# Kernel tuning notes

Measured on AMD Instinct MI355X. Metric: run time of the kernel, lower is better.

Reference implementation:

```python
import jax, jax.numpy as jnp
import numpy as np

N_NODES = 100000
N_EDGES = 2000000


def _init_mlp(key, dims, scale=0.05):
    Ws, bs = [], []
    ks = jax.random.split(key, len(dims) - 1)
    for k, di, do in zip(ks, dims[:-1], dims[1:]):
        Ws.append(jax.random.normal(k, (di, do), dtype=jnp.float32) * scale)
        bs.append(jnp.zeros((do,), dtype=jnp.float32))
    return Ws, bs


def setup_inputs() -> dict:
    key = jax.random.key(0)
    ks = jax.random.split(key, 7)
    d = {
        "t": jax.random.uniform(ks[0], (1,), dtype=jnp.float32),
        "x": jax.random.normal(ks[1], (N_NODES, 4), dtype=jnp.float32),
        "Ofixed": jax.random.normal(ks[2], (N_NODES, 2), dtype=jnp.float32),
        "src_idx": jax.random.randint(ks[3], (N_EDGES,), 0, N_NODES, dtype=jnp.int32),
        "tgt_idx": jax.random.randint(ks[4], (N_EDGES,), 0, N_NODES, dtype=jnp.int32),
    }
    # fR: (2*d_O+1)=13 -> [150]*4 -> 50 ; fO: 50 -> [100] -> 4
    R_Ws, R_bs = _init_mlp(ks[5], [13, 150, 150, 150, 150, 50])
    O_Ws, O_bs = _init_mlp(ks[6], [50, 100, 4])
    for i, (W, b) in enumerate(zip(R_Ws, R_bs)):
        d[f"fR_W{i}"] = W
        d[f"fR_b{i}"] = b
    for i, (W, b) in enumerate(zip(O_Ws, O_bs)):
        d[f"fO_W{i}"] = W
        d[f"fO_b{i}"] = b
    return d


def _mlp(h, Ws, bs):
    # hidden layers with ReLU, linear output (matches MLP in the torch code)
    for W, b in zip(Ws[:-1], bs[:-1]):
        h = jax.nn.relu(h @ W + b)
    return h @ Ws[-1] + bs[-1]


def reference(t, x, Ofixed, src_idx, tgt_idx,
              fR_W0, fR_b0, fR_W1, fR_b1, fR_W2, fR_b2, fR_W3, fR_b3, fR_W4, fR_b4,
              fO_W0, fO_b0, fO_W1, fO_b1):
    O = jnp.concatenate([x, Ofixed], axis=1)            # [N, d_O]
    # Msrc.T @ O and Mtgt.T @ O with 0/1 incidence matrices == gathers
    Rsrc = O[src_idx]                                   # [M, d_O]
    Rtgt = O[tgt_idx]                                   # [M, d_O]
    tt = jnp.broadcast_to(t.reshape(1, 1).astype(O.dtype), (src_idx.shape[0], 1))
    R_prime = jnp.concatenate([Rsrc, Rtgt, tt], axis=1)  # [M, 2*d_O+1]
    E = _mlp(R_prime, [fR_W0, fR_W1, fR_W2, fR_W3, fR_W4],
             [fR_b0, fR_b1, fR_b2, fR_b3, fR_b4])        # [M, d_E]
    # Mtgt @ E == scatter-add of edge messages onto target nodes
    E_prime = jax.ops.segment_sum(E, tgt_idx, num_segments=x.shape[0])  # [N, d_E]
    P = _mlp(E_prime, [fO_W0, fO_W1], [fO_b0, fO_b1])    # [N, d_P]
    return P
```

## Files before the change

kernel.cpp:

```cpp
#include <hip/hip_runtime.h>
#include <hip/hip_bf16.h>

typedef unsigned short u16;
typedef unsigned int u32;
typedef __attribute__((ext_vector_type(8))) short short8;
typedef __attribute__((ext_vector_type(4))) float f32x4;

constexpr int SA     = 192;
constexpr int BLK_E  = 64;
constexpr int NTHR   = 256;
constexpr int CHUNK  = 512;
constexpr int WSLOT  = 50 * CHUNK;
constexpr size_t WS_HDR   = 262144;

constexpr int Ls (int s) { return s == 0 ? 0 : (s <= 15 ? 1 + (s - 1) / 5 : 4); }
constexpr int Kss(int s) { return s == 0 ? 0 : (s <= 15 ? (s - 1) % 5 : s - 16); }

__device__ __forceinline__ int aswz(int row, int elem) {
    return row * SA + (elem ^ ((row & 7) << 3));
}

__device__ __forceinline__ u16 f2bf(float f) {
    union { float f; unsigned u; } c; c.f = f;
    return (u16)((c.u + 0x7fffu + ((c.u >> 16) & 1u)) >> 16);
}
__device__ __forceinline__ unsigned pk_bf16(float a, float b) {
    float2 f; f.x = a; f.y = b;
    __hip_bfloat162 h = __float22bfloat162_rn(f);
    return *(unsigned*)&h;
}

__device__ __forceinline__ int kperm(int kp) {
    if (kp < 64)  return (kp & 3) * 16 + (kp >> 2);
    if (kp < 128) { const int m = kp - 64; return (5 + (m & 3)) * 16 + (m >> 2); }
    if (kp < 144) return 4 * 16 + (kp - 128);
    if (kp < 160) return 9 * 16 + (kp - 144);
    return 1 << 30;
}

__global__ void prep_all(const float* __restrict__ W0, const float* __restrict__ W1,
                         const float* __restrict__ W2, const float* __restrict__ W3,
                         const float* __restrict__ W4,
                         const float* __restrict__ B0, const float* __restrict__ B1,
                         const float* __restrict__ B2, const float* __restrict__ B3,
                         const float* __restrict__ B4,
                         u16* __restrict__ Wt)
{
    const int l = blockIdx.y;
    const float* W; const float* B; int DI, DO; bool perm;
    if      (l == 0) { W = W0; B = B0; DI = 13;  DO = 150; perm = false; }
    else if (l == 1) { W = W1; B = B1; DI = 150; DO = 150; perm = true;  }
    else if (l == 2) { W = W2; B = B2; DI = 150; DO = 150; perm = true;  }
    else if (l == 3) { W = W3; B = B3; DI = 150; DO = 150; perm = true;  }
    else             { W = W4; B = B4; DI = 150; DO = 50;  perm = true;  }
    const int kbias = (l == 0) ? 13 : 150;
    u16* dst = Wt + (size_t)l * WSLOT;
    for (int idx = blockIdx.x * blockDim.x + threadIdx.x; idx < WSLOT;
         idx += gridDim.x * blockDim.x) {
        const int chunk = idx / CHUNK;
        const int within = idx - chunk * CHUNK;
        const int lane = within >> 3, e = within & 7;
        const int ks = chunk / 10, j = chunk - ks * 10;
        const int c = lane & 15, q = lane >> 4;
        const int n = j * 16 + c;
        const int kphys = ks * 32 + q * 8 + e;
        const int klog = perm ? kperm(kphys) : kphys;
        float v = 0.f;
        if (n < DO) {
            if (klog < DI)          v = W[klog * DO + n];
            else if (klog == kbias) v = B[n];
        }
        dst[idx] = f2bf(v);
    }
}

__device__ __forceinline__ void loadB(const u16* __restrict__ Wt, int s,
                                      int ng, int lane, short8 (&slot)[5])
{
    const int l = Ls(s), ks = Kss(s);
    const int jb = (l < 4) ? ng * 5 : 0;
    const int nt = (l < 4) ? 5 : 4;
    const u16* base = Wt + (size_t)l * WSLOT + (size_t)(ks * 10 + jb) * CHUNK + lane * 8;
#pragma unroll
    for (int jj = 0; jj < 5; ++jj)
        if (jj < nt) slot[jj] = *(const short8*)&base[jj * CHUNK];
}

__device__ __forceinline__ void epilogue(u16* act, int mg, int ng, int col, int quad,
                                         f32x4 (&acc)[2][5])
{
#pragma unroll
    for (int mtl = 0; mtl < 2; ++mtl)
#pragma unroll
        for (int r = 0; r < 4; ++r) {
            const int row = (mg * 2 + mtl) * 16 + quad * 4 + r;
            uint2 pk;
            pk.x = pk_bf16(fmaxf(acc[mtl][0][r], 0.f), fmaxf(acc[mtl][1][r], 0.f));
            pk.y = pk_bf16(fmaxf(acc[mtl][2][r], 0.f), fmaxf(acc[mtl][3][r], 0.f));
            *(uint2*)&act[aswz(row, ng * 64 + col * 4)] = pk;
            u16 sv = (u16)pk_bf16(fmaxf(acc[mtl][4][r], 0.f), 0.f);
            if (ng == 1 && col == 6) sv = 0x3F80;
            act[aswz(row, 128 + ng * 16 + col)] = sv;
        }
}

__global__ void hist_kernel(const int* __restrict__ tgt, u32* __restrict__ cnt,
                            int n_edges)
{
    const int e = blockIdx.x * blockDim.x + threadIdx.x;
    if (e < n_edges) atomicAdd(&cnt[tgt[e]], 1u);
}

__global__ void scan1_kernel(const u32* __restrict__ cnt, u32* __restrict__ offs,
                             u32* __restrict__ bsum, int n)
{
    __shared__ u32 s[256];
    const int i = blockIdx.x * 256 + threadIdx.x;
    const u32 v = (i < n) ? cnt[i] : 0u;
    s[threadIdx.x] = v; __syncthreads();
#pragma unroll
    for (int d = 1; d < 256; d <<= 1) {
        const u32 t = (threadIdx.x >= d) ? s[threadIdx.x - d] : 0u;
        __syncthreads();
        s[threadIdx.x] += t;
        __syncthreads();
    }
    if (i < n) offs[i] = s[threadIdx.x] - v;
    if (threadIdx.x == 255) bsum[blockIdx.x] = s[255];
}

__global__ void scan2_kernel(u32* __restrict__ bsum, int nb)
{
    __shared__ u32 s[512];
    const int i = threadIdx.x;
    const u32 v = (i < nb) ? bsum[i] : 0u;
    s[i] = v; __syncthreads();
#pragma unroll
    for (int d = 1; d < 512; d <<= 1) {
        const u32 t = (i >= d) ? s[i - d] : 0u;
        __syncthreads();
        s[i] += t;
        __syncthreads();
    }
    if (i < nb) bsum[i] = s[i] - v;
}

__global__ void scan3_kernel(u32* __restrict__ offs, const u32* __restrict__ bsum,
                             u32* __restrict__ cursor, int n, int n_edges)
{
    const int i = blockIdx.x * 256 + threadIdx.x;
    if (i < n) {
        const u32 o = offs[i] + bsum[blockIdx.x];
        offs[i] = o;
        cursor[i] = o;
    }
    if (blockIdx.x == 0 && threadIdx.x == 0) offs[n] = (u32)n_edges;
}

__global__ void perm_kernel(const int* __restrict__ src, const int* __restrict__ tgt,
                            u32* __restrict__ cursor, int2* __restrict__ sg,
                            int n_edges)
{
    const int e = blockIdx.x * blockDim.x + threadIdx.x;
    if (e < n_edges) {
        const int g = tgt[e];
        const u32 pos = atomicAdd(&cursor[g], 1u);
        sg[pos] = make_int2(src[e], g);
    }
}

__global__ __launch_bounds__(NTHR, 4) void edge_kernel(
    const float* __restrict__ t, const float* __restrict__ x, const float* __restrict__ Ofx,
    const int2* __restrict__ sgp,
    const u16* __restrict__ Wt,
    float* __restrict__ Ep, int n_edges)
{
    __shared__ __align__(16) u16 act[BLK_E * SA];
    __shared__ int tgt_s[BLK_E];

    const int tid  = threadIdx.x;
    const int lane = tid & 63;
    const int wv   = tid >> 6;
    const int mg   = wv >> 1;
    const int ng   = wv & 1;
    const int col  = lane & 15;
    const int quad = lane >> 4;

    short8 Bwin[2][5];
    loadB(Wt, 0, ng, lane, Bwin[0]);
    loadB(Wt, 1, ng, lane, Bwin[1]);

    if (lane < 16) {
        const int e = wv * 16 + lane;
        const long long ge = (long long)blockIdx.x * BLK_E + e;
        const bool valid = ge < n_edges;
        const int2 sg = valid ? sgp[ge] : make_int2(0, 0);
        const int s = sg.x;
        const int g = valid ? sg.y : -1;
        const float4 xs = valid ? *(const float4*)&x[(size_t)s * 4] : float4{0, 0, 0, 0};
        const float2 os = valid ? *(const float2*)&Ofx[(size_t)s * 2] : float2{0, 0};
        const float4 xg = valid ? *(const float4*)&x[(size_t)sg.y * 4] : float4{0, 0, 0, 0};
        const float2 og = valid ? *(const float2*)&Ofx[(size_t)sg.y * 2] : float2{0, 0};
        const float tv = valid ? t[0] : 0.f;
        uint4 w0, w1;
        w0.x = pk_bf16(xs.x, xs.y); w0.y = pk_bf16(xs.z, xs.w);
        w0.z = pk_bf16(os.x, os.y); w0.w = pk_bf16(xg.x, xg.y);
        w1.x = pk_bf16(xg.z, xg.w); w1.y = pk_bf16(og.x, og.y);
        w1.z = pk_bf16(tv, 1.0f);   w1.w = 0u;
        *(uint4*)&act[aswz(e, 0)]  = w0;
        *(uint4*)&act[aswz(e, 8)]  = w1;
        *(uint4*)&act[aswz(e, 16)] = uint4{0, 0, 0, 0};
        *(uint4*)&act[aswz(e, 24)] = uint4{0, 0, 0, 0};
        tgt_s[e] = g;
    }
    __syncthreads();

    const f32x4 z = {0.f, 0.f, 0.f, 0.f};
    f32x4 acc[2][5];
    short8 Af[2];

#pragma unroll
    for (int mtl = 0; mtl < 2; ++mtl)
        Af[mtl] = *(const short8*)&act[aswz((mg * 2 + mtl) * 16 + col, quad * 8)];
#pragma unroll
    for (int jj = 0; jj < 5; ++jj)
#pragma unroll
        for (int mtl = 0; mtl < 2; ++mtl)
            acc[mtl][jj] = __builtin_amdgcn_mfma_f32_16x16x32_bf16(
                Af[mtl], Bwin[0][jj], z, 0, 0, 0);
    loadB(Wt, 2, ng, lane, Bwin[0]);
    __syncthreads();
    epilogue(act, mg, ng, col, quad, acc);
    __syncthreads();

#pragma unroll
    for (int s = 1; s <= 15; ++s) {
        const int ks = (s - 1) % 5;
        const int slot = s & 1;
#pragma unroll
        for (int mtl = 0; mtl < 2; ++mtl)
            Af[mtl] = *(const short8*)&act[aswz((mg * 2 + mtl) * 16 + col,
                                                ks * 32 + quad * 8)];
#pragma unroll
        for (int jj = 0; jj < 5; ++jj)
#pragma unroll
            for (int mtl = 0; mtl < 2; ++mtl) {
                if (ks == 0)
                    acc[mtl][jj] = __builtin_amdgcn_mfma_f32_16x16x32_bf16(
                        Af[mtl], Bwin[slot][jj], z, 0, 0, 0);
                else
                    acc[mtl][jj] = __builtin_amdgcn_mfma_f32_16x16x32_bf16(
                        Af[mtl], Bwin[slot][jj], acc[mtl][jj], 0, 0, 0);
            }
        if (s + 2 <= 20) loadB(Wt, s + 2, ng, lane, Bwin[slot]);
        if (ks == 4) {
            __syncthreads();
            epilogue(act, mg, ng, col, quad, acc);
            __syncthreads();
        }
    }

    const int mt4 = mg * 2 + ng;
    f32x4 acc4[4];
#pragma unroll
    for (int s = 16; s <= 20; ++s) {
        const int ks = s - 16;
        const int slot = s & 1;
        const short8 A4 = *(const short8*)&act[aswz(mt4 * 16 + col,
                                                    ks * 32 + quad * 8)];
#pragma unroll
        for (int jj = 0; jj < 4; ++jj) {
            if (ks == 0)
                acc4[jj] = __builtin_amdgcn_mfma_f32_16x16x32_bf16(
                    A4, Bwin[slot][jj], z, 0, 0, 0);
            else
                acc4[jj] = __builtin_amdgcn_mfma_f32_16x16x32_bf16(
                    A4, Bwin[slot][jj], acc4[jj], 0, 0, 0);
        }
        if (s + 2 <= 20) loadB(Wt, s + 2, ng, lane, Bwin[slot]);
    }

    __syncthreads();
    float* actF = (float*)act;
#pragma unroll
    for (int jj = 0; jj < 4; ++jj) {
        const int n = jj * 16 + col;
        if (n < 50) {
#pragma unroll
            for (int r = 0; r < 4; ++r)
                actF[(mt4 * 16 + quad * 4 + r) * 52 + n] = acc4[jj][r];
        }
    }
    __syncthreads();
    if (tid < 200) {
        const int h = tid / 50;
        const int c = tid - h * 50;
        const int r0 = h * 16;
        int   cur = tgt_s[r0];
        float a   = 0.f;
        for (int r = r0; r < r0 + 16; ++r) {
            const int   g = tgt_s[r];
            const float v = actF[r * 52 + c];
            if (g != cur) {
                if (cur >= 0) atomicAdd(&Ep[(size_t)cur * 50 + c], a);
                a = 0.f; cur = g;
            }
            a += v;
        }
        if (cur >= 0) atomicAdd(&Ep[(size_t)cur * 50 + c], a);
    }
}

template<int DI, int DO, bool RELU>
__device__ __forceinline__ void mlp_layer_t(
    const float* __restrict__ W, const float* __restrict__ B,
    float (*in)[64], float (*out)[64], int tid)
{
    const int et = tid & 15;
    const int jt = tid >> 4;
    constexpr int NG = (DO + 15) / 16;

    float acc0[NG], acc1[NG], acc2[NG], acc3[NG];
#pragma unroll
    for (int g = 0; g < NG; ++g) {
        const int j = jt + 16 * g;
        const float bb = (j < DO) ? B[j] : 0.f;
        acc0[g] = bb; acc1[g] = bb; acc2[g] = bb; acc3[g] = bb;
    }
    for (int k = 0; k < DI; ++k) {
        const float4 a = *(const float4*)&in[k][et * 4];
#pragma unroll
        for (int g = 0; g < NG; ++g) {
            const int j = jt + 16 * g;
            const float wv = (j < DO) ? W[k * DO + j] : 0.f;
            acc0[g] = fmaf(a.x, wv, acc0[g]);
            acc1[g] = fmaf(a.y, wv, acc1[g]);
            acc2[g] = fmaf(a.z, wv, acc2[g]);
            acc3[g] = fmaf(a.w, wv, acc3[g]);
        }
    }
#pragma unroll
    for (int g = 0; g < NG; ++g) {
        const int j = jt + 16 * g;
        if (j < DO) {
            float4 v; v.x = acc0[g]; v.y = acc1[g]; v.z = acc2[g]; v.w = acc3[g];
            if (RELU) {
                v.x = fmaxf(v.x, 0.f); v.y = fmaxf(v.y, 0.f);
                v.z = fmaxf(v.z, 0.f); v.w = fmaxf(v.w, 0.f);
            }
            *(float4*)&out[j][et * 4] = v;
        }
    }
}

__global__ __launch_bounds__(256, 2) void node_kernel(
    const float* __restrict__ Ep,
    const float* __restrict__ W0, const float* __restrict__ B0,
    const float* __restrict__ W1, const float* __restrict__ B1,
    float* __restrict__ P, int n_nodes)
{
    __shared__ float bufA[104][64];
    __shared__ float bufB[104][64];
    const int tid = threadIdx.x;
    const int n0  = blockIdx.x * 64;

    for (int idx = tid; idx < 64 * 50; idx += 256) {
        const int e = idx / 50;
        const int k = idx - e * 50;
        const int n = n0 + e;
        bufA[k][e] = (n < n_nodes) ? Ep[(size_t)n * 50 + k] : 0.f;
    }
    __syncthreads();
    mlp_layer_t<50, 100, true >(W0, B0, bufA, bufB, tid); __syncthreads();
    mlp_layer_t<100, 4, false>(W1, B1, bufB, bufA, tid); __syncthreads();
    for (int idx = tid; idx < 64 * 4; idx += 256) {
        const int e = idx & 63;
        const int j = idx >> 6;
        const int n = n0 + e;
        if (n < n_nodes) P[(size_t)n * 4 + j] = bufA[j][e];
    }
}

extern "C" void kernel_launch(void* const* d_in, const int* in_sizes, int n_in,
                              void* d_out, int out_size, void* d_ws, size_t ws_size,
                              hipStream_t stream)
{
    const float* t   = (const float*)d_in[0];
    const float* x   = (const float*)d_in[1];
    const float* Ofx = (const float*)d_in[2];
    const int*   src = (const int*)d_in[3];
    const int*   tgt = (const int*)d_in[4];
    const float* W0  = (const float*)d_in[5];  const float* B0 = (const float*)d_in[6];
    const float* W1  = (const float*)d_in[7];  const float* B1 = (const float*)d_in[8];
    const float* W2  = (const float*)d_in[9];  const float* B2 = (const float*)d_in[10];
    const float* W3  = (const float*)d_in[11]; const float* B3 = (const float*)d_in[12];
    const float* W4  = (const float*)d_in[13]; const float* B4 = (const float*)d_in[14];
    const float* OW0 = (const float*)d_in[15]; const float* OB0 = (const float*)d_in[16];
    const float* OW1 = (const float*)d_in[17]; const float* OB1 = (const float*)d_in[18];

    const int n_nodes = in_sizes[1] / 4;
    const int n_edges = in_sizes[3];

    auto align256 = [](size_t v) { return (v + 255) & ~(size_t)255; };
    char* ws = (char*)d_ws;
    const size_t copy_elems = (size_t)n_nodes * 50;
    size_t o = 0;
    u16*   Wt       = (u16*)(ws + o);  o = WS_HDR;
    float* Ep       = (float*)(ws + o); o = align256(o + copy_elems * sizeof(float));
    u32*   offs     = (u32*)(ws + o);  o = align256(o + (size_t)(n_nodes + 1) * 4);
    u32*   cursor   = (u32*)(ws + o);  o = align256(o + (size_t)n_nodes * 4);
    u32*   bsum     = (u32*)(ws + o);  o = align256(o + 512 * 4);
    int2*  sg_perm  = (int2*)(ws + o); o = align256(o + (size_t)n_edges * 8);

    const int NB  = (n_nodes + 255) / 256;
    const int EBK = (n_edges + 255) / 256;

    prep_all<<<dim3(32, 5), 256, 0, stream>>>(W0, W1, W2, W3, W4,
                                              B0, B1, B2, B3, B4, Wt);
    hipMemsetAsync(Ep, 0, copy_elems * sizeof(float), stream);
    hipMemsetAsync(cursor, 0, (size_t)n_nodes * 4, stream);

    hist_kernel <<<EBK, 256, 0, stream>>>(tgt, cursor, n_edges);
    scan1_kernel<<<NB, 256, 0, stream>>>(cursor, offs, bsum, n_nodes);
    scan2_kernel<<<1, 512, 0, stream>>>(bsum, NB);
    scan3_kernel<<<NB, 256, 0, stream>>>(offs, bsum, cursor, n_nodes, n_edges);
    perm_kernel <<<EBK, 256, 0, stream>>>(src, tgt, cursor, sg_perm, n_edges);

    edge_kernel<<<(n_edges + BLK_E - 1) / BLK_E, NTHR, 0, stream>>>(
        t, x, Ofx, sg_perm, Wt, Ep, n_edges);

    node_kernel<<<(n_nodes + 63) / 64, 256, 0, stream>>>(
        Ep, OW0, OB0, OW1, OB1, (float*)d_out, n_nodes);
}
```

Baseline: 907.2 us.

## Stage MLP weights in LDS via async loads and double edges per block

Each wave previously loaded its own slice of weight tiles from global memory into registers. The kernel now uses global_load_lds to stream each weight k-slice once per block into a double-buffered LDS area that all waves read. The block also grows to 128 edges and 512 threads, so each weight fetch is spread over more edges. In exchange there is a block-wide barrier every k-step and more LDS per block, which can lower occupancy. Correctness also depends on the async LDS writes being complete before the barrier.

```diff
diff --git a/kernel.cpp b/kernel.cpp
--- a/kernel.cpp
+++ b/kernel.cpp
@@ -7,8 +7,8 @@
 typedef __attribute__((ext_vector_type(4))) float f32x4;
 
 constexpr int SA     = 192;
-constexpr int BLK_E  = 64;
-constexpr int NTHR   = 256;
+constexpr int BLK_E  = 128;
+constexpr int NTHR   = 512;
 constexpr int CHUNK  = 512;
 constexpr int WSLOT  = 50 * CHUNK;
 constexpr size_t WS_HDR   = 262144;
@@ -28,6 +28,12 @@
     float2 f; f.x = a; f.y = b;
     __hip_bfloat162 h = __float22bfloat162_rn(f);
     return *(unsigned*)&h;
+}
+
+typedef __attribute__((address_space(3))) u16 as3_u16;
+typedef const __attribute__((address_space(1))) u16 as1_u16;
+__device__ __forceinline__ void async16(u16* lds_dst, const u16* gsrc) {
+    __builtin_amdgcn_global_load_lds((as1_u16*)gsrc, (as3_u16*)lds_dst, 16, 0, 0);
 }
 
 __device__ __forceinline__ int kperm(int kp) {
@@ -74,18 +80,6 @@
     }
 }
 
-__device__ __forceinline__ void loadB(const u16* __restrict__ Wt, int s,
-                                      int ng, int lane, short8 (&slot)[5])
-{
-    const int l = Ls(s), ks = Kss(s);
-    const int jb = (l < 4) ? ng * 5 : 0;
-    const int nt = (l < 4) ? 5 : 4;
-    const u16* base = Wt + (size_t)l * WSLOT + (size_t)(ks * 10 + jb) * CHUNK + lane * 8;
-#pragma unroll
-    for (int jj = 0; jj < 5; ++jj)
-        if (jj < nt) slot[jj] = *(const short8*)&base[jj * CHUNK];
-}
-
 __device__ __forceinline__ void epilogue(u16* act, int mg, int ng, int col, int quad,
                                          f32x4 (&acc)[2][5])
 {
@@ -176,6 +170,7 @@
     float* __restrict__ Ep, int n_edges)
 {
     __shared__ __align__(16) u16 act[BLK_E * SA];
+    __shared__ __align__(16) u16 Bs[2][10 * CHUNK];
     __shared__ int tgt_s[BLK_E];
 
     const int tid  = threadIdx.x;
@@ -185,10 +180,14 @@
     const int ng   = wv & 1;
     const int col  = lane & 15;
     const int quad = lane >> 4;
-
-    short8 Bwin[2][5];
-    loadB(Wt, 0, ng, lane, Bwin[0]);
-    loadB(Wt, 1, ng, lane, Bwin[1]);
+    const int jb   = ng * 5;
+
+    {
+        const u16* base = Wt;
+        async16(&Bs[0][wv * CHUNK], base + wv * CHUNK + lane * 8);
+        if (wv < 2)
+            async16(&Bs[0][(8 + wv) * CHUNK], base + (8 + wv) * CHUNK + lane * 8);
+    }
 
     if (lane < 16) {
         const int e = wv * 16 + lane;
@@ -217,26 +216,25 @@
 
     const f32x4 z = {0.f, 0.f, 0.f, 0.f};
     f32x4 acc[2][5];
-    short8 Af[2];
-
-#pragma unroll
-    for (int mtl = 0; mtl < 2; ++mtl)
-        Af[mtl] = *(const short8*)&act[aswz((mg * 2 + mtl) * 16 + col, quad * 8)];
-#pragma unroll
-    for (int jj = 0; jj < 5; ++jj)
-#pragma unroll
-        for (int mtl = 0; mtl < 2; ++mtl)
-            acc[mtl][jj] = __builtin_amdgcn_mfma_f32_16x16x32_bf16(
-                Af[mtl], Bwin[0][jj], z, 0, 0, 0);
-    loadB(Wt, 2, ng, lane, Bwin[0]);
-    __syncthreads();
-    epilogue(act, mg, ng, col, quad, acc);
-    __syncthreads();
-
-#pragma unroll
-    for (int s = 1; s <= 15; ++s) {
-        const int ks = (s - 1) % 5;
-        const int slot = s & 1;
+    short8 Af[2], Bc[5];
+
+#pragma unroll
+    for (int s = 0; s <= 15; ++s) {
+        const int ks = Kss(s);
+        const bool first = (s == 0) || (ks == 0);
+        const bool last  = (s == 0) || (ks == 4);
+        {
+            const int sn = s + 1;
+            const u16* base = Wt + (size_t)Ls(sn) * WSLOT
+                                 + (size_t)(Kss(sn) * 10) * CHUNK;
+            u16* bd = &Bs[sn & 1][0];
+            async16(&bd[wv * CHUNK], base + wv * CHUNK + lane * 8);
+            if (wv < 2)
+                async16(&bd[(8 + wv) * CHUNK], base + (8 + wv) * CHUNK + lane * 8);
+        }
+#pragma unroll
+        for (int jj = 0; jj < 5; ++jj)
+            Bc[jj] = *(const short8*)&Bs[s & 1][(jb + jj) * CHUNK + lane * 8];
 #pragma unroll
         for (int mtl = 0; mtl < 2; ++mtl)
             Af[mtl] = *(const short8*)&act[aswz((mg * 2 + mtl) * 16 + col,
@@ -245,42 +243,52 @@
         for (int jj = 0; jj < 5; ++jj)
 #pragma unroll
             for (int mtl = 0; mtl < 2; ++mtl) {
-                if (ks == 0)
+                if (first)
                     acc[mtl][jj] = __builtin_amdgcn_mfma_f32_16x16x32_bf16(
-                        Af[mtl], Bwin[slot][jj], z, 0, 0, 0);
+                        Af[mtl], Bc[jj], z, 0, 0, 0);
                 else
                     acc[mtl][jj] = __builtin_amdgcn_mfma_f32_16x16x32_bf16(
-                        Af[mtl], Bwin[slot][jj], acc[mtl][jj], 0, 0, 0);
+                        Af[mtl], Bc[jj], acc[mtl][jj], 0, 0, 0);
             }
-        if (s + 2 <= 20) loadB(Wt, s + 2, ng, lane, Bwin[slot]);
-        if (ks == 4) {
-            __syncthreads();
+        __syncthreads();
+        if (last) {
             epilogue(act, mg, ng, col, quad, acc);
             __syncthreads();
         }
     }
 
-    const int mt4 = mg * 2 + ng;
+    const int mt4 = wv;
     f32x4 acc4[4];
 #pragma unroll
     for (int s = 16; s <= 20; ++s) {
         const int ks = s - 16;
-        const int slot = s & 1;
+        if (s < 20) {
+            const int sn = s + 1;
+            const u16* base = Wt + (size_t)4 * WSLOT
+                                 + (size_t)(Kss(sn) * 10) * CHUNK;
+            u16* bd = &Bs[sn & 1][0];
+            async16(&bd[wv * CHUNK], base + wv * CHUNK + lane * 8);
+            if (wv < 2)
+                async16(&bd[(8 + wv) * CHUNK], base + (8 + wv) * CHUNK + lane * 8);
+        }
+        short8 B4[4];
+#pragma unroll
+        for (int jj = 0; jj < 4; ++jj)
+            B4[jj] = *(const short8*)&Bs[s & 1][jj * CHUNK + lane * 8];
         const short8 A4 = *(const short8*)&act[aswz(mt4 * 16 + col,
                                                     ks * 32 + quad * 8)];
 #pragma unroll
         for (int jj = 0; jj < 4; ++jj) {
             if (ks == 0)
                 acc4[jj] = __builtin_amdgcn_mfma_f32_16x16x32_bf16(
-                    A4, Bwin[slot][jj], z, 0, 0, 0);
+                    A4, B4[jj], z, 0, 0, 0);
             else
                 acc4[jj] = __builtin_amdgcn_mfma_f32_16x16x32_bf16(
-                    A4, Bwin[slot][jj], acc4[jj], 0, 0, 0);
-        }
-        if (s + 2 <= 20) loadB(Wt, s + 2, ng, lane, Bwin[slot]);
-    }
-
-    __syncthreads();
+                    A4, B4[jj], acc4[jj], 0, 0, 0);
+        }
+        __syncthreads();
+    }
+
     float* actF = (float*)act;
 #pragma unroll
     for (int jj = 0; jj < 4; ++jj) {
@@ -292,7 +300,7 @@
         }
     }
     __syncthreads();
-    if (tid < 200) {
+    if (tid < 400) {
         const int h = tid / 50;
         const int c = tid - h * 50;
         const int r0 = h * 16;
```

Measured after the change: 903.6 us. Within noise of the previous version (-0.4%).

## Make each wave own 32 edges with full-width layers, removing block barriers

Applied to the files above, without the earlier changes.

Reorganizes the edge MLP so each wavefront processes its own 32 edges across all 160 output columns, instead of splitting N across wave pairs. This eliminates all __syncthreads between layers, since each wave reads and writes only its own rows in LDS. The block size doubles to 128 edges, and the accumulator count doubles to 20 f32x4 per thread, so launch bounds drop to 3 blocks per SM. Each wave now loads the full weight tiles itself, which doubles per-wave weight traffic and raises register pressure and LDS use.

```diff
diff --git a/kernel.cpp b/kernel.cpp
--- a/kernel.cpp
+++ b/kernel.cpp
@@ -7,7 +7,7 @@
 typedef __attribute__((ext_vector_type(4))) float f32x4;
 
 constexpr int SA     = 192;
-constexpr int BLK_E  = 64;
+constexpr int BLK_E  = 128;
 constexpr int NTHR   = 256;
 constexpr int CHUNK  = 512;
 constexpr int WSLOT  = 50 * CHUNK;
@@ -74,33 +74,37 @@
     }
 }
 
-__device__ __forceinline__ void loadB(const u16* __restrict__ Wt, int s,
-                                      int ng, int lane, short8 (&slot)[5])
-{
-    const int l = Ls(s), ks = Kss(s);
-    const int jb = (l < 4) ? ng * 5 : 0;
-    const int nt = (l < 4) ? 5 : 4;
-    const u16* base = Wt + (size_t)l * WSLOT + (size_t)(ks * 10 + jb) * CHUNK + lane * 8;
+__device__ __forceinline__ void loadHalf(const u16* __restrict__ Wt,
+                                         int l, int ks, int g, int nch,
+                                         int lane, short8* buf)
+{
+    const u16* base = Wt + (size_t)l * WSLOT + (size_t)(ks * 10 + g * 5) * CHUNK
+                         + lane * 8;
 #pragma unroll
     for (int jj = 0; jj < 5; ++jj)
-        if (jj < nt) slot[jj] = *(const short8*)&base[jj * CHUNK];
-}
-
-__device__ __forceinline__ void epilogue(u16* act, int mg, int ng, int col, int quad,
-                                         f32x4 (&acc)[2][5])
+        if (jj < nch) buf[jj] = *(const short8*)&base[jj * CHUNK];
+}
+
+__device__ __forceinline__ void epilogueF(u16* act, int ebase, int col, int quad,
+                                          f32x4 (&acc)[2][10])
 {
 #pragma unroll
     for (int mtl = 0; mtl < 2; ++mtl)
 #pragma unroll
         for (int r = 0; r < 4; ++r) {
-            const int row = (mg * 2 + mtl) * 16 + quad * 4 + r;
-            uint2 pk;
-            pk.x = pk_bf16(fmaxf(acc[mtl][0][r], 0.f), fmaxf(acc[mtl][1][r], 0.f));
-            pk.y = pk_bf16(fmaxf(acc[mtl][2][r], 0.f), fmaxf(acc[mtl][3][r], 0.f));
-            *(uint2*)&act[aswz(row, ng * 64 + col * 4)] = pk;
-            u16 sv = (u16)pk_bf16(fmaxf(acc[mtl][4][r], 0.f), 0.f);
-            if (ng == 1 && col == 6) sv = 0x3F80;
-            act[aswz(row, 128 + ng * 16 + col)] = sv;
+            const int row = ebase + mtl * 16 + quad * 4 + r;
+            uint2 p0, p1;
+            p0.x = pk_bf16(fmaxf(acc[mtl][0][r], 0.f), fmaxf(acc[mtl][1][r], 0.f));
+            p0.y = pk_bf16(fmaxf(acc[mtl][2][r], 0.f), fmaxf(acc[mtl][3][r], 0.f));
+            p1.x = pk_bf16(fmaxf(acc[mtl][5][r], 0.f), fmaxf(acc[mtl][6][r], 0.f));
+            p1.y = pk_bf16(fmaxf(acc[mtl][7][r], 0.f), fmaxf(acc[mtl][8][r], 0.f));
+            *(uint2*)&act[aswz(row, col * 4)]      = p0;
+            *(uint2*)&act[aswz(row, 64 + col * 4)] = p1;
+            act[aswz(row, 128 + col)] =
+                (u16)pk_bf16(fmaxf(acc[mtl][4][r], 0.f), 0.f);
+            u16 sv = (u16)pk_bf16(fmaxf(acc[mtl][9][r], 0.f), 0.f);
+            if (col == 6) sv = 0x3F80;
+            act[aswz(row, 144 + col)] = sv;
         }
 }
 
@@ -169,7 +173,7 @@
     }
 }
 
-__global__ __launch_bounds__(NTHR, 4) void edge_kernel(
+__global__ __launch_bounds__(NTHR, 3) void edge_kernel(
     const float* __restrict__ t, const float* __restrict__ x, const float* __restrict__ Ofx,
     const int2* __restrict__ sgp,
     const u16* __restrict__ Wt,
@@ -178,27 +182,21 @@
     __shared__ __align__(16) u16 act[BLK_E * SA];
     __shared__ int tgt_s[BLK_E];
 
-    const int tid  = threadIdx.x;
-    const int lane = tid & 63;
-    const int wv   = tid >> 6;
-    const int mg   = wv >> 1;
-    const int ng   = wv & 1;
-    const int col  = lane & 15;
-    const int quad = lane >> 4;
-
-    short8 Bwin[2][5];
-    loadB(Wt, 0, ng, lane, Bwin[0]);
-    loadB(Wt, 1, ng, lane, Bwin[1]);
-
-    if (lane < 16) {
-        const int e = wv * 16 + lane;
+    const int tid   = threadIdx.x;
+    const int lane  = tid & 63;
+    const int wv    = tid >> 6;
+    const int ebase = wv * 32;
+    const int col   = lane & 15;
+    const int quad  = lane >> 4;
+
+    if (lane < 32) {
+        const int e = ebase + lane;
         const long long ge = (long long)blockIdx.x * BLK_E + e;
         const bool valid = ge < n_edges;
         const int2 sg = valid ? sgp[ge] : make_int2(0, 0);
-        const int s = sg.x;
         const int g = valid ? sg.y : -1;
-        const float4 xs = valid ? *(const float4*)&x[(size_t)s * 4] : float4{0, 0, 0, 0};
-        const float2 os = valid ? *(const float2*)&Ofx[(size_t)s * 2] : float2{0, 0};
+        const float4 xs = valid ? *(const float4*)&x[(size_t)sg.x * 4] : float4{0, 0, 0, 0};
+        const float2 os = valid ? *(const float2*)&Ofx[(size_t)sg.x * 2] : float2{0, 0};
         const float4 xg = valid ? *(const float4*)&x[(size_t)sg.y * 4] : float4{0, 0, 0, 0};
         const float2 og = valid ? *(const float2*)&Ofx[(size_t)sg.y * 2] : float2{0, 0};
         const float tv = valid ? t[0] : 0.f;
@@ -213,93 +211,77 @@
         *(uint4*)&act[aswz(e, 24)] = uint4{0, 0, 0, 0};
         tgt_s[e] = g;
     }
-    __syncthreads();
 
     const f32x4 z = {0.f, 0.f, 0.f, 0.f};
-    f32x4 acc[2][5];
+    f32x4 acc[2][10];
+    short8 Wb[2][5];
     short8 Af[2];
 
+    loadHalf(Wt, 0, 0, 0, 5, lane, Wb[0]);
+    loadHalf(Wt, 0, 0, 1, 5, lane, Wb[1]);
+
+#pragma unroll
+    for (int s = 0; s <= 15; ++s) {
+        const int ks = Kss(s);
+        const bool first = (s == 0) || (ks == 0);
+#pragma unroll
+        for (int mtl = 0; mtl < 2; ++mtl)
+            Af[mtl] = *(const short8*)&act[aswz(ebase + mtl * 16 + col,
+                                                ks * 32 + quad * 8)];
+#pragma unroll
+        for (int jj = 0; jj < 5; ++jj)
+#pragma unroll
+            for (int mtl = 0; mtl < 2; ++mtl)
+                acc[mtl][jj] = __builtin_amdgcn_mfma_f32_16x16x32_bf16(
+                    Af[mtl], Wb[0][jj], first ? z : acc[mtl][jj], 0, 0, 0);
+        if (s < 15) loadHalf(Wt, Ls(s + 1), Kss(s + 1), 0, 5, lane, Wb[0]);
+        else        loadHalf(Wt, 4, 0, 0, 4, lane, Wb[0]);
+#pragma unroll
+        for (int jj = 0; jj < 5; ++jj)
+#pragma unroll
+            for (int mtl = 0; mtl < 2; ++mtl)
+                acc[mtl][5 + jj] = __builtin_amdgcn_mfma_f32_16x16x32_bf16(
+                    Af[mtl], Wb[1][jj], first ? z : acc[mtl][5 + jj], 0, 0, 0);
+        if (s < 15) loadHalf(Wt, Ls(s + 1), Kss(s + 1), 1, 5, lane, Wb[1]);
+        else        loadHalf(Wt, 4, 1, 0, 4, lane, Wb[1]);
+        if (s == 0 || ks == 4)
+            epilogueF(act, ebase, col, quad, acc);
+    }
+
+    f32x4 acc4[2][4];
+#pragma unroll
+    for (int ks = 0; ks < 5; ++ks) {
+#pragma unroll
+        for (int mtl = 0; mtl < 2; ++mtl)
+            Af[mtl] = *(const short8*)&act[aswz(ebase + mtl * 16 + col,
+                                                ks * 32 + quad * 8)];
+#pragma unroll
+        for (int jj = 0; jj < 4; ++jj)
+#pragma unroll
+            for (int mtl = 0; mtl < 2; ++mtl)
+                acc4[mtl][jj] = __builtin_amdgcn_mfma_f32_16x16x32_bf16(
+                    Af[mtl], Wb[ks & 1][jj], (ks == 0) ? z : acc4[mtl][jj], 0, 0, 0);
+        if (ks + 2 <= 4) loadHalf(Wt, 4, ks + 2, 0, 4, lane, Wb[ks & 1]);
+    }
+
+    float* actF = (float*)&act[ebase * SA];
 #pragma unroll
     for (int mtl = 0; mtl < 2; ++mtl)
-        Af[mtl] = *(const short8*)&act[aswz((mg * 2 + mtl) * 16 + col, quad * 8)];
-#pragma unroll
-    for (int jj = 0; jj < 5; ++jj)
-#pragma unroll
-        for (int mtl = 0; mtl < 2; ++mtl)
-            acc[mtl][jj] = __builtin_amdgcn_mfma_f32_16x16x32_bf16(
-                Af[mtl], Bwin[0][jj], z, 0, 0, 0);
-    loadB(Wt, 2, ng, lane, Bwin[0]);
-    __syncthreads();
-    epilogue(act, mg, ng, col, quad, acc);
-    __syncthreads();
-
-#pragma unroll
-    for (int s = 1; s <= 15; ++s) {
-        const int ks = (s - 1) % 5;
-        const int slot = s & 1;
-#pragma unroll
-        for (int mtl = 0; mtl < 2; ++mtl)
-            Af[mtl] = *(const short8*)&act[aswz((mg * 2 + mtl) * 16 + col,
-                                                ks * 32 + quad * 8)];
-#pragma unroll
-        for (int jj = 0; jj < 5; ++jj)
-#pragma unroll
-            for (int mtl = 0; mtl < 2; ++mtl) {
-                if (ks == 0)
-                    acc[mtl][jj] = __builtin_amdgcn_mfma_f32_16x16x32_bf16(
-                        Af[mtl], Bwin[slot][jj], z, 0, 0, 0);
-                else
-                    acc[mtl][jj] = __builtin_amdgcn_mfma_f32_16x16x32_bf16(
-                        Af[mtl], Bwin[slot][jj], acc[mtl][jj], 0, 0, 0);
+#pragma unroll
+        for (int jj = 0; jj < 4; ++jj) {
+            const int n = jj * 16 + col;
+            if (n < 50) {
+#pragma unroll
+                for (int r = 0; r < 4; ++r)
+                    actF[(mtl * 16 + quad * 4 + r) * 52 + n] = acc4[mtl][jj][r];
             }
-        if (s + 2 <= 20) loadB(Wt, s + 2, ng, lane, Bwin[slot]);
-        if (ks == 4) {
-            __syncthreads();
-            epilogue(act, mg, ng, col, quad, acc);
-            __syncthreads();
-        }
-    }
-
-    const int mt4 = mg * 2 + ng;
-    f32x4 acc4[4];
-#pragma unroll
-    for (int s = 16; s <= 20; ++s) {
-        const int ks = s - 16;
-        const int slot = s & 1;
-        const short8 A4 = *(const short8*)&act[aswz(mt4 * 16 + col,
-                                                    ks * 32 + quad * 8)];
-#pragma unroll
-        for (int jj = 0; jj < 4; ++jj) {
-            if (ks == 0)
-                acc4[jj] = __builtin_amdgcn_mfma_f32_16x16x32_bf16(
-                    A4, Bwin[slot][jj], z, 0, 0, 0);
-            else
-                acc4[jj] = __builtin_amdgcn_mfma_f32_16x16x32_bf16(
-                    A4, Bwin[slot][jj], acc4[jj], 0, 0, 0);
-        }
-        if (s + 2 <= 20) loadB(Wt, s + 2, ng, lane, Bwin[slot]);
-    }
-
-    __syncthreads();
-    float* actF = (float*)act;
-#pragma unroll
-    for (int jj = 0; jj < 4; ++jj) {
-        const int n = jj * 16 + col;
-        if (n < 50) {
-#pragma unroll
-            for (int r = 0; r < 4; ++r)
-                actF[(mt4 * 16 + quad * 4 + r) * 52 + n] = acc4[jj][r];
-        }
-    }
-    __syncthreads();
-    if (tid < 200) {
-        const int h = tid / 50;
-        const int c = tid - h * 50;
-        const int r0 = h * 16;
-        int   cur = tgt_s[r0];
+        }
+    if (lane < 50) {
+        const int c = lane;
+        int   cur = tgt_s[ebase];
         float a   = 0.f;
-        for (int r = r0; r < r0 + 16; ++r) {
-            const int   g = tgt_s[r];
+        for (int r = 0; r < 32; ++r) {
+            const int   g = tgt_s[ebase + r];
             const float v = actF[r * 52 + c];
             if (g != cur) {
                 if (cur >= 0) atomicAdd(&Ep[(size_t)cur * 50 + c], a);
```

Result: faster. 884.9 us (-2.5%).
